# Performance work log

Hardware: AMD Instinct MI355X
Metric: run time of the kernel (lower is better)

The kernel has to match this reference:

```python
import jax, jax.numpy as jnp
import numpy as np

N_NODES = 50000
N_EDGES = 800000
IN_F = 128
OUT_F = 256


def setup_inputs() -> dict:
    key = jax.random.key(0)
    k1, k2, k3, k4, k5, k6 = jax.random.split(key, 6)
    x = jax.random.normal(k1, (N_NODES, IN_F), dtype=jnp.float32)
    edge_row = jax.random.randint(k2, (N_EDGES,), 0, N_NODES, dtype=jnp.int32)
    edge_col = jax.random.randint(k3, (N_EDGES,), 0, N_NODES, dtype=jnp.int32)
    edge_val = jax.random.uniform(k4, (N_EDGES,), dtype=jnp.float32)
    weight = jax.random.normal(k5, (IN_F, OUT_F), dtype=jnp.float32) * (1.0 / np.sqrt(OUT_F))
    b = jax.random.normal(k6, (OUT_F,), dtype=jnp.float32) * 0.01
    return {"x": x, "edge_row": edge_row, "edge_col": edge_col,
            "edge_val": edge_val, "weight": weight, "b": b}


def reference(x, edge_row, edge_col, edge_val, weight, b):
    # spmm: agg[i] = sum_{e: row[e]==i} val[e] * x[col[e]]
    msgs = edge_val[:, None] * x[edge_col]              # [E, in_f]
    agg = jax.ops.segment_sum(msgs, edge_row, num_segments=x.shape[0])  # [N, in_f]
    # dense transform + bias
    return agg @ weight + b                              # [N, out_f]
```

## Files before the change

kernel.cpp:

```cpp
#include <hip/hip_runtime.h>

#define N_NODES 50000
#define N_EDGES 800000
#define IN_F    128
#define OUT_F   256


__global__ __launch_bounds__(256)
void hist_rank(const int* __restrict__ row, int* __restrict__ cnt,
               int* __restrict__ rank, int E) {
    int e = blockIdx.x * blockDim.x + threadIdx.x;
    if (e < E) rank[e] = atomicAdd(&cnt[row[e]], 1);
}

#define SCAN_BLK 1024

__global__ __launch_bounds__(SCAN_BLK)
void scan_block(const int* __restrict__ cnt, int* __restrict__ rptr,
                int* __restrict__ bsum, int n) {
    __shared__ int s[SCAN_BLK];
    const int gid = blockIdx.x * SCAN_BLK + threadIdx.x;
    const int v = (gid < n) ? cnt[gid] : 0;
    s[threadIdx.x] = v;
    __syncthreads();
    for (int d = 1; d < SCAN_BLK; d <<= 1) {
        int t = (threadIdx.x >= d) ? s[threadIdx.x - d] : 0;
        __syncthreads();
        s[threadIdx.x] += t;
        __syncthreads();
    }
    const int incl = s[threadIdx.x];
    if (gid < n) rptr[gid] = incl - v;
    if (threadIdx.x == SCAN_BLK - 1) bsum[blockIdx.x] = incl;
}

__global__ __launch_bounds__(64)
void scan_top(int* __restrict__ bsum, int nb) {
    const int lane = threadIdx.x;
    int v = (lane < nb) ? bsum[lane] : 0;
    for (int d = 1; d < 64; d <<= 1) {
        int u = __shfl_up(v, d);
        if (lane >= d) v += u;
    }
    int ex = __shfl_up(v, 1);
    if (lane == 0) ex = 0;
    if (lane < nb) bsum[lane] = ex;
}

__global__ __launch_bounds__(SCAN_BLK)
void scan_add(int* __restrict__ rptr, const int* __restrict__ bsum, int n) {
    const int gid = blockIdx.x * SCAN_BLK + threadIdx.x;
    if (gid < n) rptr[gid] += bsum[blockIdx.x];
}

__global__ __launch_bounds__(256)
void edge_fill(const int* __restrict__ row, const int* __restrict__ col,
               const float* __restrict__ val,
               const int* __restrict__ rptr, const int* __restrict__ rank,
               unsigned long long* __restrict__ recs, int E) {
    int e = blockIdx.x * blockDim.x + threadIdx.x;
    if (e >= E) return;
    const int r = row[e];
    const int p = rptr[r] + rank[e];
    const unsigned long long rec =
        ((unsigned long long)__float_as_uint(val[e]) << 32) | (unsigned)col[e];
    recs[p] = rec;
}

__global__ __launch_bounds__(256)
void gather_agg(const float* __restrict__ x,
                const int*   __restrict__ rptr,
                const int*   __restrict__ cnt,
                const unsigned long long* __restrict__ recs,
                float*       __restrict__ out,
                int M) {
    const int wave = threadIdx.x >> 6;
    const int lane = threadIdx.x & 63;
    const int node = blockIdx.x * 4 + wave;
    if (node >= M) return;

    const int es = lane >> 3;
    const int fg = lane & 7;

    const int st = rptr[node];
    const int d  = cnt[node];

    float acc[16];
#pragma unroll
    for (int i = 0; i < 16; ++i) acc[i] = 0.f;

    for (int j0 = 0; j0 < d; j0 += 8) {
        const int  idx = j0 + es;
        const bool ok  = (idx < d);
        const unsigned long long rec = recs[st + (ok ? idx : 0)];
        const int   c = (int)(unsigned)(rec & 0xffffffffull);
        const float v = ok ? __uint_as_float((unsigned)(rec >> 32)) : 0.f;

        const float4* xp = reinterpret_cast<const float4*>(
            x + (size_t)c * IN_F + fg * 16);
        const float4 x0 = xp[0], x1 = xp[1], x2 = xp[2], x3 = xp[3];

        acc[0]  += v * x0.x; acc[1]  += v * x0.y; acc[2]  += v * x0.z; acc[3]  += v * x0.w;
        acc[4]  += v * x1.x; acc[5]  += v * x1.y; acc[6]  += v * x1.z; acc[7]  += v * x1.w;
        acc[8]  += v * x2.x; acc[9]  += v * x2.y; acc[10] += v * x2.z; acc[11] += v * x2.w;
        acc[12] += v * x3.x; acc[13] += v * x3.y; acc[14] += v * x3.z; acc[15] += v * x3.w;
    }

#pragma unroll
    for (int i = 0; i < 16; ++i) {
        acc[i] += __shfl_xor(acc[i], 8);
        acc[i] += __shfl_xor(acc[i], 16);
        acc[i] += __shfl_xor(acc[i], 32);
    }

    if (es == 0) {
        float* op = out + (size_t)node * OUT_F + fg * 16;
        reinterpret_cast<float4*>(op)[0] = make_float4(acc[0],  acc[1],  acc[2],  acc[3]);
        reinterpret_cast<float4*>(op)[1] = make_float4(acc[4],  acc[5],  acc[6],  acc[7]);
        reinterpret_cast<float4*>(op)[2] = make_float4(acc[8],  acc[9],  acc[10], acc[11]);
        reinterpret_cast<float4*>(op)[3] = make_float4(acc[12], acc[13], acc[14], acc[15]);
    }
}

#define GM 32
#define KC 32

__global__ __launch_bounds__(256)
void gemm_bias(const float* __restrict__ W,
               const float* __restrict__ bias,
               float*       __restrict__ out,
               int M) {
    __shared__ float sA[GM][IN_F];
    __shared__ float sW[KC][OUT_F];

    const int tid = threadIdx.x;
    const int r0  = blockIdx.x * GM;

#pragma unroll
    for (int i = 0; i < 4; ++i) {
        const int fi = tid + i * 256;
        const int r  = fi >> 5;
        const int q  = fi & 31;
        const int gr = r0 + r;
        const float4 v = (gr < M)
            ? *reinterpret_cast<const float4*>(out + (size_t)gr * OUT_F + q * 4)
            : make_float4(0.f, 0.f, 0.f, 0.f);
        *reinterpret_cast<float4*>(&sA[r][q * 4]) = v;
    }

    const int c4 = tid & 63;
    const int ty = tid >> 6;

    float acc[8][4];
#pragma unroll
    for (int i = 0; i < 8; ++i)
#pragma unroll
        for (int j = 0; j < 4; ++j) acc[i][j] = 0.f;

    for (int k0 = 0; k0 < IN_F; k0 += KC) {
#pragma unroll
        for (int i = 0; i < 8; ++i) {
            const int fi = tid + i * 256;
            const int kk = fi >> 6;
            const int c  = fi & 63;
            *reinterpret_cast<float4*>(&sW[kk][c * 4]) =
                *reinterpret_cast<const float4*>(W + (size_t)(k0 + kk) * OUT_F + c * 4);
        }
        __syncthreads();

#pragma unroll 8
        for (int kk = 0; kk < KC; ++kk) {
            const float4 w = *reinterpret_cast<const float4*>(&sW[kk][c4 * 4]);
#pragma unroll
            for (int i = 0; i < 8; ++i) {
                const float a = sA[ty * 8 + i][k0 + kk];
                acc[i][0] += a * w.x;
                acc[i][1] += a * w.y;
                acc[i][2] += a * w.z;
                acc[i][3] += a * w.w;
            }
        }
        __syncthreads();
    }

    const float4 bv = *reinterpret_cast<const float4*>(bias + c4 * 4);
#pragma unroll
    for (int i = 0; i < 8; ++i) {
        const int gr = r0 + ty * 8 + i;
        if (gr < M) {
            const float4 o = make_float4(acc[i][0] + bv.x, acc[i][1] + bv.y,
                                         acc[i][2] + bv.z, acc[i][3] + bv.w);
            *reinterpret_cast<float4*>(out + (size_t)gr * OUT_F + c4 * 4) = o;
        }
    }
}

extern "C" void kernel_launch(void* const* d_in, const int* in_sizes, int n_in,
                              void* d_out, int out_size, void* d_ws, size_t ws_size,
                              hipStream_t stream) {
    const float* x        = (const float*)d_in[0];
    const int*   edge_row = (const int*)  d_in[1];
    const int*   edge_col = (const int*)  d_in[2];
    const float* edge_val = (const float*)d_in[3];
    const float* weight   = (const float*)d_in[4];
    const float* bias     = (const float*)d_in[5];
    float* out = (float*)d_out;

    int* cnt  = (int*)d_ws;
    int* rptr = cnt + 50000;
    int* bsum = rptr + 50000;
    int* rank = bsum + 64;
    unsigned long long* recs = (unsigned long long*)(rank + 800000);

    hipMemsetAsync(cnt, 0, (size_t)N_NODES * sizeof(int), stream);

    const int nscan = (N_NODES + SCAN_BLK - 1) / SCAN_BLK;

    hist_rank<<<(N_EDGES + 255) / 256, 256, 0, stream>>>(edge_row, cnt, rank, N_EDGES);
    scan_block<<<nscan, SCAN_BLK, 0, stream>>>(cnt, rptr, bsum, N_NODES);
    scan_top<<<1, 64, 0, stream>>>(bsum, nscan);
    scan_add<<<nscan, SCAN_BLK, 0, stream>>>(rptr, bsum, N_NODES);
    edge_fill<<<(N_EDGES + 255) / 256, 256, 0, stream>>>(
        edge_row, edge_col, edge_val, rptr, rank, recs, N_EDGES);

    gather_agg<<<(N_NODES + 3) / 4, 256, 0, stream>>>(
        x, rptr, cnt, recs, out, N_NODES);

    gemm_bias<<<(N_NODES + GM - 1) / GM, 256, 0, stream>>>(
        weight, bias, out, N_NODES);
}
```

Measured before the change: 249.9 us.

## Use bf16 features for gather and MFMA bf16 GEMM for the transform

Converts x to bf16 in a pre-pass so the per-edge gather reads half the bytes, and stores the aggregated rows as bf16 in the output buffer. The fp32 shared-memory GEMM is replaced by an MFMA 16x16x32 bf16 kernel that loads A fragments straight from the bf16 intermediate and reads B from a transposed bf16 weight copy. This cuts gather bandwidth and moves the dense transform onto matrix cores. In exchange it adds two conversion kernels and lowers precision from fp32 to bf16 on both inputs and intermediates.

```diff
diff --git a/kernel.cpp b/kernel.cpp
--- a/kernel.cpp
+++ b/kernel.cpp
@@ -1,10 +1,49 @@
 #include <hip/hip_runtime.h>
+#include <hip/hip_bf16.h>
 
 #define N_NODES 50000
 #define N_EDGES 800000
 #define IN_F    128
 #define OUT_F   256
 
+typedef __attribute__((ext_vector_type(8))) short  short8;
+typedef __attribute__((ext_vector_type(4))) float  f32x4;
+
+static __device__ __forceinline__ unsigned short f2bf(float f) {
+    __hip_bfloat16 h = __float2bfloat16(f);
+    return *reinterpret_cast<unsigned short*>(&h);
+}
+
+
+__global__ __launch_bounds__(256)
+void convert_x(const float* __restrict__ x, unsigned short* __restrict__ xb, int n8) {
+    const int i = blockIdx.x * blockDim.x + threadIdx.x;
+    if (i >= n8) return;
+    const float4* xp = reinterpret_cast<const float4*>(x) + (size_t)i * 2;
+    const float4 a = xp[0], b = xp[1];
+    uint4 o;
+    o.x = (unsigned)f2bf(a.x) | ((unsigned)f2bf(a.y) << 16);
+    o.y = (unsigned)f2bf(a.z) | ((unsigned)f2bf(a.w) << 16);
+    o.z = (unsigned)f2bf(b.x) | ((unsigned)f2bf(b.y) << 16);
+    o.w = (unsigned)f2bf(b.z) | ((unsigned)f2bf(b.w) << 16);
+    reinterpret_cast<uint4*>(xb)[i] = o;
+}
+
+__global__ __launch_bounds__(256)
+void convert_w(const float* __restrict__ W, unsigned short* __restrict__ Wt) {
+    const int n  = blockIdx.x * 16 + (threadIdx.x & 15);
+    const int kc = threadIdx.x >> 4;
+    unsigned q[4];
+#pragma unroll
+    for (int j = 0; j < 4; ++j) {
+        const int k = kc * 8 + j * 2;
+        const unsigned short u0 = f2bf(W[(size_t)k * OUT_F + n]);
+        const unsigned short u1 = f2bf(W[(size_t)(k + 1) * OUT_F + n]);
+        q[j] = (unsigned)u0 | ((unsigned)u1 << 16);
+    }
+    *reinterpret_cast<uint4*>(Wt + (size_t)n * IN_F + kc * 8) =
+        make_uint4(q[0], q[1], q[2], q[3]);
+}
 
 __global__ __launch_bounds__(256)
 void hist_rank(const int* __restrict__ row, int* __restrict__ cnt,
@@ -68,12 +107,11 @@
 }
 
 __global__ __launch_bounds__(256)
-void gather_agg(const float* __restrict__ x,
-                const int*   __restrict__ rptr,
-                const int*   __restrict__ cnt,
+void gather_agg(const unsigned short* __restrict__ xb,
+                const int* __restrict__ rptr,
+                const int* __restrict__ cnt,
                 const unsigned long long* __restrict__ recs,
-                float*       __restrict__ out,
-                int M) {
+                float* __restrict__ out, int M) {
     const int wave = threadIdx.x >> 6;
     const int lane = threadIdx.x & 63;
     const int node = blockIdx.x * 4 + wave;
@@ -96,14 +134,15 @@
         const int   c = (int)(unsigned)(rec & 0xffffffffull);
         const float v = ok ? __uint_as_float((unsigned)(rec >> 32)) : 0.f;
 
-        const float4* xp = reinterpret_cast<const float4*>(
-            x + (size_t)c * IN_F + fg * 16);
-        const float4 x0 = xp[0], x1 = xp[1], x2 = xp[2], x3 = xp[3];
-
-        acc[0]  += v * x0.x; acc[1]  += v * x0.y; acc[2]  += v * x0.z; acc[3]  += v * x0.w;
-        acc[4]  += v * x1.x; acc[5]  += v * x1.y; acc[6]  += v * x1.z; acc[7]  += v * x1.w;
-        acc[8]  += v * x2.x; acc[9]  += v * x2.y; acc[10] += v * x2.z; acc[11] += v * x2.w;
-        acc[12] += v * x3.x; acc[13] += v * x3.y; acc[14] += v * x3.z; acc[15] += v * x3.w;
+        const uint4* xp = reinterpret_cast<const uint4*>(
+            xb + (size_t)c * IN_F + fg * 16);
+        const uint4 a = xp[0], b = xp[1];
+        const unsigned w[8] = {a.x, a.y, a.z, a.w, b.x, b.y, b.z, b.w};
+#pragma unroll
+        for (int j = 0; j < 8; ++j) {
+            acc[2 * j]     += v * __uint_as_float(w[j] << 16);
+            acc[2 * j + 1] += v * __uint_as_float(w[j] & 0xffff0000u);
+        }
     }
 
 #pragma unroll
@@ -114,83 +153,81 @@
     }
 
     if (es == 0) {
-        float* op = out + (size_t)node * OUT_F + fg * 16;
-        reinterpret_cast<float4*>(op)[0] = make_float4(acc[0],  acc[1],  acc[2],  acc[3]);
-        reinterpret_cast<float4*>(op)[1] = make_float4(acc[4],  acc[5],  acc[6],  acc[7]);
-        reinterpret_cast<float4*>(op)[2] = make_float4(acc[8],  acc[9],  acc[10], acc[11]);
-        reinterpret_cast<float4*>(op)[3] = make_float4(acc[12], acc[13], acc[14], acc[15]);
-    }
-}
-
-#define GM 32
-#define KC 32
-
-__global__ __launch_bounds__(256)
-void gemm_bias(const float* __restrict__ W,
+        unsigned q[8];
+#pragma unroll
+        for (int j = 0; j < 8; ++j)
+            q[j] = (unsigned)f2bf(acc[2 * j]) | ((unsigned)f2bf(acc[2 * j + 1]) << 16);
+        unsigned short* op =
+            reinterpret_cast<unsigned short*>(out) + (size_t)node * 512 + fg * 16;
+        reinterpret_cast<uint4*>(op)[0] = make_uint4(q[0], q[1], q[2], q[3]);
+        reinterpret_cast<uint4*>(op)[1] = make_uint4(q[4], q[5], q[6], q[7]);
+    }
+}
+
+__global__ __launch_bounds__(256)
+void gemm_mfma(const unsigned short* __restrict__ Wt,
                const float* __restrict__ bias,
-               float*       __restrict__ out,
-               int M) {
-    __shared__ float sA[GM][IN_F];
-    __shared__ float sW[KC][OUT_F];
-
+               float* __restrict__ out, int M) {
     const int tid = threadIdx.x;
-    const int r0  = blockIdx.x * GM;
-
-#pragma unroll
-    for (int i = 0; i < 4; ++i) {
-        const int fi = tid + i * 256;
-        const int r  = fi >> 5;
-        const int q  = fi & 31;
-        const int gr = r0 + r;
-        const float4 v = (gr < M)
-            ? *reinterpret_cast<const float4*>(out + (size_t)gr * OUT_F + q * 4)
-            : make_float4(0.f, 0.f, 0.f, 0.f);
-        *reinterpret_cast<float4*>(&sA[r][q * 4]) = v;
-    }
-
-    const int c4 = tid & 63;
-    const int ty = tid >> 6;
-
-    float acc[8][4];
-#pragma unroll
-    for (int i = 0; i < 8; ++i)
-#pragma unroll
-        for (int j = 0; j < 4; ++j) acc[i][j] = 0.f;
-
-    for (int k0 = 0; k0 < IN_F; k0 += KC) {
-#pragma unroll
-        for (int i = 0; i < 8; ++i) {
-            const int fi = tid + i * 256;
-            const int kk = fi >> 6;
-            const int c  = fi & 63;
-            *reinterpret_cast<float4*>(&sW[kk][c * 4]) =
-                *reinterpret_cast<const float4*>(W + (size_t)(k0 + kk) * OUT_F + c * 4);
-        }
-        __syncthreads();
-
-#pragma unroll 8
-        for (int kk = 0; kk < KC; ++kk) {
-            const float4 w = *reinterpret_cast<const float4*>(&sW[kk][c4 * 4]);
-#pragma unroll
-            for (int i = 0; i < 8; ++i) {
-                const float a = sA[ty * 8 + i][k0 + kk];
-                acc[i][0] += a * w.x;
-                acc[i][1] += a * w.y;
-                acc[i][2] += a * w.z;
-                acc[i][3] += a * w.w;
+    const int wv  = tid >> 6;
+    const int l   = tid & 63;
+    const int wvm = wv >> 1, wvn = wv & 1;
+    const int lr  = l & 15;
+    const int lg  = l >> 4;
+    const int r0  = blockIdx.x * 64;
+
+    short8 af[2][4];
+#pragma unroll
+    for (int mt = 0; mt < 2; ++mt) {
+        const int row = r0 + wvm * 32 + mt * 16 + lr;
+        const unsigned short* ap =
+            reinterpret_cast<const unsigned short*>(out) + (size_t)row * 512;
+#pragma unroll
+        for (int kk = 0; kk < 4; ++kk) {
+            short8 v = {0, 0, 0, 0, 0, 0, 0, 0};
+            if (row < M)
+                v = *reinterpret_cast<const short8*>(ap + kk * 32 + lg * 8);
+            af[mt][kk] = v;
+        }
+    }
+    __syncthreads();
+
+    f32x4 acc[2][8];
+#pragma unroll
+    for (int mt = 0; mt < 2; ++mt)
+#pragma unroll
+        for (int nt = 0; nt < 8; ++nt) acc[mt][nt] = (f32x4){0.f, 0.f, 0.f, 0.f};
+
+#pragma unroll
+    for (int kk = 0; kk < 4; ++kk) {
+        short8 bf[8];
+#pragma unroll
+        for (int nt = 0; nt < 8; ++nt) {
+            const int colc = wvn * 128 + nt * 16 + lr;
+            bf[nt] = *reinterpret_cast<const short8*>(
+                Wt + (size_t)colc * IN_F + kk * 32 + lg * 8);
+        }
+#pragma unroll
+        for (int mt = 0; mt < 2; ++mt)
+#pragma unroll
+            for (int nt = 0; nt < 8; ++nt)
+                acc[mt][nt] = __builtin_amdgcn_mfma_f32_16x16x32_bf16(
+                    af[mt][kk], bf[nt], acc[mt][nt], 0, 0, 0);
+    }
+
+#pragma unroll
+    for (int nt = 0; nt < 8; ++nt) {
+        const int colc = wvn * 128 + nt * 16 + lr;
+        const float bv = bias[colc];
+#pragma unroll
+        for (int mt = 0; mt < 2; ++mt) {
+            const int rbase = r0 + wvm * 32 + mt * 16 + lg * 4;
+#pragma unroll
+            for (int r = 0; r < 4; ++r) {
+                const int gr = rbase + r;
+                if (gr < M)
+                    out[(size_t)gr * OUT_F + colc] = acc[mt][nt][r] + bv;
             }
-        }
-        __syncthreads();
-    }
-
-    const float4 bv = *reinterpret_cast<const float4*>(bias + c4 * 4);
-#pragma unroll
-    for (int i = 0; i < 8; ++i) {
-        const int gr = r0 + ty * 8 + i;
-        if (gr < M) {
-            const float4 o = make_float4(acc[i][0] + bv.x, acc[i][1] + bv.y,
-                                         acc[i][2] + bv.z, acc[i][3] + bv.w);
-            *reinterpret_cast<float4*>(out + (size_t)gr * OUT_F + c4 * 4) = o;
         }
     }
 }
@@ -206,16 +243,22 @@
     const float* bias     = (const float*)d_in[5];
     float* out = (float*)d_out;
 
-    int* cnt  = (int*)d_ws;
+    char* w = (char*)d_ws;
+    unsigned short* xb = (unsigned short*)w;
+    unsigned long long* recs = (unsigned long long*)(w + 12800000);
+    unsigned short* Wt = (unsigned short*)(w + 19200000);
+    int* cnt  = (int*)(w + 19265536);
     int* rptr = cnt + 50000;
     int* bsum = rptr + 50000;
     int* rank = bsum + 64;
-    unsigned long long* recs = (unsigned long long*)(rank + 800000);
 
     hipMemsetAsync(cnt, 0, (size_t)N_NODES * sizeof(int), stream);
 
+    convert_x<<<(N_NODES * IN_F / 8 + 255) / 256, 256, 0, stream>>>(
+        x, xb, N_NODES * IN_F / 8);
+    convert_w<<<16, 256, 0, stream>>>(weight, Wt);
+
     const int nscan = (N_NODES + SCAN_BLK - 1) / SCAN_BLK;
-
     hist_rank<<<(N_EDGES + 255) / 256, 256, 0, stream>>>(edge_row, cnt, rank, N_EDGES);
     scan_block<<<nscan, SCAN_BLK, 0, stream>>>(cnt, rptr, bsum, N_NODES);
     scan_top<<<1, 64, 0, stream>>>(bsum, nscan);
@@ -224,8 +267,8 @@
         edge_row, edge_col, edge_val, rptr, rank, recs, N_EDGES);
 
     gather_agg<<<(N_NODES + 3) / 4, 256, 0, stream>>>(
-        x, rptr, cnt, recs, out, N_NODES);
-
-    gemm_bias<<<(N_NODES + GM - 1) / GM, 256, 0, stream>>>(
-        weight, bias, out, N_NODES);
-}
+        xb, rptr, cnt, recs, out, N_NODES);
+
+    gemm_mfma<<<(N_NODES + 63) / 64, 256, 0, stream>>>(
+        Wt, bias, out, N_NODES);
+}
```

Result: faster. 219.4 us (-12.2%).
